# Kernel optimization log

Hardware: AMD Instinct MI355X
Metric: run time of the kernel (lower is better)

## Reference

```python
import jax, jax.numpy as jnp
import numpy as np

VOCAB = 50257
B, V, HID, OUT = 32, 1024, 768, 256


def setup_inputs() -> dict:
    key = jax.random.key(0)
    k1, k2, k3, k4, k5 = jax.random.split(key, 5)
    emb_table = jax.random.normal(k1, (VOCAB, HID), dtype=jnp.float32) * 0.02
    adj = jax.random.uniform(k2, (B, V, V), dtype=jnp.float32)
    fc_w = jax.random.normal(k3, (OUT, HID), dtype=jnp.float32) * (1.0 / np.sqrt(HID))
    fc_b = jax.random.normal(k4, (OUT,), dtype=jnp.float32) * 0.01
    gv_ids = jax.random.randint(k5, (B, V), 0, VOCAB, dtype=jnp.int64)
    return {"emb_table": emb_table, "adj": adj, "fc_w": fc_w, "fc_b": fc_b, "gv_ids": gv_ids}


def reference(emb_table, adj, fc_w, fc_b, gv_ids):
    # Per-sample embedding gather: [B, V, HID]
    gvocab_ev = emb_table[gv_ids]
    # adj @ E, then mean over node rows -> fuse: sum over both node axes / V
    # H_vh = adj[b] @ E[b]  (V,V)@(V,HID); graph_embed = H_vh.mean(axis=0)
    h = jnp.einsum('bvw,bwh->bh', adj, gvocab_ev) / V  # [B, HID]
    # fc_hg linear (activation=None, dropout disabled)
    out = h @ fc_w.T + fc_b  # [B, OUT]
    return out
```

## Files before the change

kernel.cpp:

```cpp
#include <hip/hip_runtime.h>

#define B   32
#define V   1024
#define HID 768
#define OUT 256

__global__ void colsum_kernel(const float* __restrict__ adj, float* __restrict__ c) {
    const int b   = blockIdx.x;
    const int vc  = blockIdx.y;
    const int tid = threadIdx.x;
    const float4* adj4 = reinterpret_cast<const float4*>(adj) + (size_t)b * V * (V / 4);
    float4 acc = make_float4(0.f, 0.f, 0.f, 0.f);
    const int v0 = vc * 64;
    #pragma unroll 4
    for (int v = v0; v < v0 + 64; ++v) {
        float4 a = adj4[(size_t)v * (V / 4) + tid];
        acc.x += a.x; acc.y += a.y; acc.z += a.z; acc.w += a.w;
    }
    float* cb = c + b * V + tid * 4;
    atomicAdd(cb + 0, acc.x);
    atomicAdd(cb + 1, acc.y);
    atomicAdd(cb + 2, acc.z);
    atomicAdd(cb + 3, acc.w);
}

__global__ void gather_wsum_kernel(const float* __restrict__ emb,
                                   const int* __restrict__ ids,
                                   const float* __restrict__ c,
                                   float* __restrict__ h) {
    const int b   = blockIdx.x;
    const int wc  = blockIdx.y;
    const int tid = threadIdx.x;
    __shared__ int   ids_s[64];
    __shared__ float c_s[64];
    if (tid < 64) {
        ids_s[tid] = ids[b * V + wc * 64 + tid];
        c_s[tid]   = c[b * V + wc * 64 + tid];
    }
    __syncthreads();
    float a0 = 0.f, a1 = 0.f, a2 = 0.f;
    #pragma unroll 2
    for (int i = 0; i < 64; ++i) {
        const float* T = emb + (size_t)ids_s[i] * HID;
        const float  s = c_s[i];
        a0 += s * T[tid];
        a1 += s * T[tid + 256];
        a2 += s * T[tid + 512];
    }
    atomicAdd(h + b * HID + tid,       a0);
    atomicAdd(h + b * HID + tid + 256, a1);
    atomicAdd(h + b * HID + tid + 512, a2);
}

__global__ void fc_kernel(const float* __restrict__ h,
                          const float* __restrict__ fc_w,
                          const float* __restrict__ fc_b,
                          float* __restrict__ out) {
    const int b    = blockIdx.x;
    const int wave = threadIdx.x >> 6;
    const int lane = threadIdx.x & 63;
    const int o    = blockIdx.y * 4 + wave;
    __shared__ float h_s[HID];
    for (int i = threadIdx.x; i < HID; i += 256) h_s[i] = h[b * HID + i];
    __syncthreads();
    const float* wrow = fc_w + (size_t)o * HID;
    float acc = 0.f;
    #pragma unroll
    for (int k = 0; k < HID / 64; ++k)
        acc += wrow[k * 64 + lane] * h_s[k * 64 + lane];
    #pragma unroll
    for (int off = 32; off > 0; off >>= 1)
        acc += __shfl_down(acc, off, 64);
    if (lane == 0)
        out[b * OUT + o] = fc_b[o] + acc * (1.0f / V);
}

extern "C" void kernel_launch(void* const* d_in, const int* in_sizes, int n_in,
                              void* d_out, int out_size, void* d_ws, size_t ws_size,
                              hipStream_t stream) {
    const float* emb  = (const float*)d_in[0];
    const float* adj  = (const float*)d_in[1];
    const float* fc_w = (const float*)d_in[2];
    const float* fc_b = (const float*)d_in[3];
    const int*   ids  = (const int*)d_in[4];
    float* out = (float*)d_out;

    float* c = (float*)d_ws;
    float* h = c + B * V;

    hipMemsetAsync(d_ws, 0, (size_t)(B * V + B * HID) * sizeof(float), stream);

    colsum_kernel<<<dim3(B, 16), 256, 0, stream>>>(adj, c);
    gather_wsum_kernel<<<dim3(B, 16), 256, 0, stream>>>(emb, ids, c, h);
    fc_kernel<<<dim3(B, OUT / 4), 256, 0, stream>>>(h, fc_w, fc_b, out);
}
```

Baseline: 59.75 us.

## Drop memset and atomics in column sum; vectorize gather with finer split

The column-sum kernel now gives each block a 64-column strip over all V rows. Partials are reduced in shared memory and written directly, so the c atomics go away. The same kernel also zeroes h, which removes the separate memset launch. The gather kernel uses float4 loads with 192 threads and splits the rows into 32 chunks instead of 16. The cost is that each column-sum block now reads only 256 bytes per row, a narrower access pattern that may hurt DRAM efficiency.

```diff
diff --git a/kernel.cpp b/kernel.cpp
--- a/kernel.cpp
+++ b/kernel.cpp
@@ -5,51 +5,55 @@
 #define HID 768
 #define OUT 256
 
-__global__ void colsum_kernel(const float* __restrict__ adj, float* __restrict__ c) {
-    const int b   = blockIdx.x;
-    const int vc  = blockIdx.y;
-    const int tid = threadIdx.x;
-    const float4* adj4 = reinterpret_cast<const float4*>(adj) + (size_t)b * V * (V / 4);
-    float4 acc = make_float4(0.f, 0.f, 0.f, 0.f);
-    const int v0 = vc * 64;
-    #pragma unroll 4
-    for (int v = v0; v < v0 + 64; ++v) {
-        float4 a = adj4[(size_t)v * (V / 4) + tid];
-        acc.x += a.x; acc.y += a.y; acc.z += a.z; acc.w += a.w;
-    }
-    float* cb = c + b * V + tid * 4;
-    atomicAdd(cb + 0, acc.x);
-    atomicAdd(cb + 1, acc.y);
-    atomicAdd(cb + 2, acc.z);
-    atomicAdd(cb + 3, acc.w);
+__global__ void colsum_kernel(const float* __restrict__ adj,
+                              float* __restrict__ c,
+                              float* __restrict__ h) {
+    const int b  = blockIdx.x;
+    const int wc = blockIdx.y;
+    const int t  = threadIdx.x;
+    const int wi = t & 63;
+    const int vo = t >> 6;
+    const float* base = adj + (size_t)b * V * V + wc * 64 + wi;
+    float acc = 0.f;
+    #pragma unroll 8
+    for (int v = vo; v < V; v += 4)
+        acc += base[(size_t)v * V];
+    __shared__ float sm[4][64];
+    sm[vo][wi] = acc;
+    __syncthreads();
+    if (t < 64)
+        c[b * V + wc * 64 + t] = sm[0][t] + sm[1][t] + sm[2][t] + sm[3][t];
+    if (wc < 3)
+        h[b * HID + wc * 256 + t] = 0.f;
 }
 
 __global__ void gather_wsum_kernel(const float* __restrict__ emb,
                                    const int* __restrict__ ids,
                                    const float* __restrict__ c,
                                    float* __restrict__ h) {
-    const int b   = blockIdx.x;
-    const int wc  = blockIdx.y;
-    const int tid = threadIdx.x;
-    __shared__ int   ids_s[64];
-    __shared__ float c_s[64];
-    if (tid < 64) {
-        ids_s[tid] = ids[b * V + wc * 64 + tid];
-        c_s[tid]   = c[b * V + wc * 64 + tid];
+    const int b  = blockIdx.x;
+    const int wc = blockIdx.y;
+    const int t  = threadIdx.x;
+    __shared__ int   ids_s[32];
+    __shared__ float c_s[32];
+    if (t < 32) {
+        ids_s[t] = ids[b * V + wc * 32 + t];
+        c_s[t]   = c[b * V + wc * 32 + t];
     }
     __syncthreads();
-    float a0 = 0.f, a1 = 0.f, a2 = 0.f;
-    #pragma unroll 2
-    for (int i = 0; i < 64; ++i) {
-        const float* T = emb + (size_t)ids_s[i] * HID;
+    float4 acc = make_float4(0.f, 0.f, 0.f, 0.f);
+    #pragma unroll 4
+    for (int i = 0; i < 32; ++i) {
+        const float4* T4 = reinterpret_cast<const float4*>(emb + (size_t)ids_s[i] * HID);
+        const float4 a = T4[t];
         const float  s = c_s[i];
-        a0 += s * T[tid];
-        a1 += s * T[tid + 256];
-        a2 += s * T[tid + 512];
+        acc.x += s * a.x; acc.y += s * a.y; acc.z += s * a.z; acc.w += s * a.w;
     }
-    atomicAdd(h + b * HID + tid,       a0);
-    atomicAdd(h + b * HID + tid + 256, a1);
-    atomicAdd(h + b * HID + tid + 512, a2);
+    float* hb = h + b * HID + t * 4;
+    atomicAdd(hb + 0, acc.x);
+    atomicAdd(hb + 1, acc.y);
+    atomicAdd(hb + 2, acc.z);
+    atomicAdd(hb + 3, acc.w);
 }
 
 __global__ void fc_kernel(const float* __restrict__ h,
@@ -88,9 +92,7 @@
     float* c = (float*)d_ws;
     float* h = c + B * V;
 
-    hipMemsetAsync(d_ws, 0, (size_t)(B * V + B * HID) * sizeof(float), stream);
-
-    colsum_kernel<<<dim3(B, 16), 256, 0, stream>>>(adj, c);
-    gather_wsum_kernel<<<dim3(B, 16), 256, 0, stream>>>(emb, ids, c, h);
+    colsum_kernel<<<dim3(B, 16), 256, 0, stream>>>(adj, c, h);
+    gather_wsum_kernel<<<dim3(B, 32), 192, 0, stream>>>(emb, ids, c, h);
     fc_kernel<<<dim3(B, OUT / 4), 256, 0, stream>>>(h, fc_w, fc_b, out);
 }
```

Result: slower. 67.71 us (+13.3%).
